# Optimization experiments

Measured on AMD Instinct MI355X. Metric: run time of the kernel, lower is better.

## Reference

```python
import jax, jax.numpy as jnp
import numpy as np

N, F, R, H, C = 16384, 128, 16, 8, 64
E = 163840
SELF_LOOP_FILL = 0.5
NEG_SLOPE = 0.2


def _glorot(key, shape):
    fan = shape[0] + shape[-1]
    lim = jnp.sqrt(6.0 / fan)
    return jax.random.uniform(key, shape, jnp.float32, -lim, lim)


def setup_inputs() -> dict:
    key = jax.random.key(0)
    ks = jax.random.split(key, 20)
    inp = {
        'x': jax.random.normal(ks[0], (N, F), jnp.float32),
        'edge_index': jax.random.randint(ks[1], (2, E), 0, N, jnp.int64),
        'edge_attr': jax.random.uniform(ks[2], (E, R), jnp.float32),
        # layer 1 (concat=True): in=F, out per head=C, heads=H
        'Wl1': _glorot(ks[3], (F, H * C)), 'bl1': jnp.zeros((H * C,), jnp.float32),
        'Wr1': _glorot(ks[4], (F, H * C)), 'br1': jnp.zeros((H * C,), jnp.float32),
        'We1': _glorot(ks[5], (R, H * C)),
        'att1': _glorot(ks[6], (H, C)),
        'bias1': jnp.zeros((H * C,), jnp.float32),
        # layer 2 (concat=False): in=H*C
        'Wl2': _glorot(ks[7], (H * C, H * C)), 'bl2': jnp.zeros((H * C,), jnp.float32),
        'Wr2': _glorot(ks[8], (H * C, H * C)), 'br2': jnp.zeros((H * C,), jnp.float32),
        'We2': _glorot(ks[9], (R, H * C)),
        'att2': _glorot(ks[10], (H, C)),
        'bias2': jnp.zeros((C,), jnp.float32),
    }
    return inp


def gatv2_layer(x, src, dst, e, Wl, bl, Wr, br, We, att, bias, concat):
    n = x.shape[0]
    h, c = att.shape
    xl = (x @ Wl + bl).reshape(n, h, c)   # source transform (used for messages)
    xr = (x @ Wr + br).reshape(n, h, c)   # target transform
    ep = (e @ We).reshape(-1, h, c)       # edge feature transform [E',H,C]
    z = jax.nn.leaky_relu(xl[src] + xr[dst] + ep, NEG_SLOPE)  # [E',H,C]
    logits = jnp.einsum('ehc,hc->eh', z, att)                 # [E',H]
    # softmax over incoming edges of each destination node
    m = jax.ops.segment_max(logits, dst, num_segments=n)
    m = jax.lax.stop_gradient(jnp.where(jnp.isfinite(m), m, 0.0))
    ex = jnp.exp(logits - m[dst])
    denom = jax.ops.segment_sum(ex, dst, num_segments=n)
    alpha = ex / (denom[dst] + 1e-16)                         # [E',H]
    out = jax.ops.segment_sum(xl[src] * alpha[..., None], dst, num_segments=n)  # [N,H,C]
    out = out.reshape(n, h * c) if concat else out.mean(axis=1)
    return out + bias


def reference(x, edge_index, edge_attr, Wl1, bl1, Wr1, br1, We1, att1, bias1,
              Wl2, bl2, Wr2, br2, We2, att2, bias2):
    n = x.shape[0]
    loops = jnp.arange(n, dtype=edge_index.dtype)
    src = jnp.concatenate([edge_index[0], loops])
    dst = jnp.concatenate([edge_index[1], loops])
    e = jnp.concatenate([edge_attr, jnp.full((n, edge_attr.shape[1]), SELF_LOOP_FILL, edge_attr.dtype)])
    out = gatv2_layer(x, src, dst, e, Wl1, bl1, Wr1, br1, We1, att1, bias1, concat=True)
    out = gatv2_layer(out, src, dst, e, Wl2, bl2, Wr2, br2, We2, att2, bias2, concat=False)
    return out
```

## Files before the change

### kernel.cpp

```cpp
#include <hip/hip_runtime.h>
#include <cstdint>

#define NN 16384
#define FF 128
#define RR 16
#define HH 8
#define CC 64
#define HC 512
#define NC 1024
#define EE 163840
#define ET (EE + NN)

typedef __attribute__((ext_vector_type(4))) float f32x4;
typedef __attribute__((ext_vector_type(8))) short short8;

__device__ __forceinline__ unsigned short f2bf(float f) {
  unsigned u = __builtin_bit_cast(unsigned, f);
  u = (u + 0x7FFFu + ((u >> 16) & 1u)) >> 16;
  return (unsigned short)u;
}
__device__ __forceinline__ float bf2f(unsigned short b) {
  unsigned u = ((unsigned)b) << 16;
  return __builtin_bit_cast(float, u);
}

__device__ __forceinline__ void gl_lds16(const void* g, void* l) {
  __builtin_amdgcn_global_load_lds(
      (const __attribute__((address_space(1))) unsigned int*)g,
      (__attribute__((address_space(3))) unsigned int*)l, 16, 0, 0);
}

__global__ __launch_bounds__(256) void count_kernel(const int* __restrict__ ei,
                                                    int* __restrict__ counts) {
  int e = blockIdx.x * 256 + threadIdx.x;
  if (e >= ET) return;
  int d = (e < EE) ? ei[EE + e] : (e - EE);
  atomicAdd(&counts[d], 1);
}

__global__ __launch_bounds__(1024) void scan_kernel(const int* __restrict__ counts,
                                                    int* __restrict__ offs,
                                                    int* __restrict__ cursor) {
  __shared__ int part[1024];
  int t = threadIdx.x;
  int base = t * 16;
  int loc[16];
  int s = 0;
#pragma unroll
  for (int i = 0; i < 16; ++i) { loc[i] = s; s += counts[base + i]; }
  part[t] = s;
  __syncthreads();
  for (int off = 1; off < 1024; off <<= 1) {
    int v = (t >= off) ? part[t - off] : 0;
    __syncthreads();
    part[t] += v;
    __syncthreads();
  }
  int excl = part[t] - s;
#pragma unroll
  for (int i = 0; i < 16; ++i) {
    int o = excl + loc[i];
    offs[base + i] = o;
    cursor[base + i] = o;
  }
  if (t == 1023) offs[NN] = part[1023];
}

__global__ __launch_bounds__(256) void scatter_kernel(const int* __restrict__ ei,
                                                      int* __restrict__ cursor,
                                                      int* __restrict__ csr,
                                                      int* __restrict__ srcc,
                                                      int* __restrict__ dstc) {
  int e = blockIdx.x * 256 + threadIdx.x;
  if (e >= ET) return;
  int s, d;
  if (e < EE) { s = ei[e]; d = ei[EE + e]; }
  else        { s = d = e - EE; }
  int p = atomicAdd(&cursor[d], 1);
  csr[p] = e;
  srcc[p] = s;
  dstc[p] = d;
}

__global__ __launch_bounds__(256) void pack_a_kernel(const float* __restrict__ A,
                                                     unsigned short* __restrict__ Ah,
                                                     unsigned short* __restrict__ Al,
                                                     int K) {
  int nkb = K >> 5;
  int rb = blockIdx.x / nkb, kb = blockIdx.x % nkb;
  int t = threadIdx.x;
  size_t obase = ((size_t)rb * nkb + kb) * 4096;
#pragma unroll
  for (int u = 0; u < 2; ++u) {
    int lin = t + u * 256;
    int r = lin >> 2, ch = lin & 3;
    int chs = (ch + (r >> 1)) & 3;
    const float* src = &A[(size_t)(rb * 128 + r) * K + kb * 32 + ch * 8];
    float4 v0 = *(const float4*)src;
    float4 v1 = *(const float4*)(src + 4);
    float v[8] = {v0.x, v0.y, v0.z, v0.w, v1.x, v1.y, v1.z, v1.w};
    short8 hv, lv;
#pragma unroll
    for (int j = 0; j < 8; ++j) {
      unsigned short h = f2bf(v[j]);
      unsigned short l = f2bf(v[j] - bf2f(h));
      hv[j] = (short)h; lv[j] = (short)l;
    }
    size_t o = obase + (size_t)r * 32 + chs * 8;
    *(short8*)&Ah[o] = hv;
    *(short8*)&Al[o] = lv;
  }
}

__global__ __launch_bounds__(256) void pack_w_kernel(const float* __restrict__ Wl,
                                                     const float* __restrict__ Wr,
                                                     unsigned short* __restrict__ Bh,
                                                     unsigned short* __restrict__ Bl,
                                                     int K) {
  int nkb = K >> 5;
  int nb = blockIdx.x / nkb, kb = blockIdx.x % nkb;
  int t = threadIdx.x;
  size_t obase = ((size_t)nb * nkb + kb) * 4096;
#pragma unroll
  for (int u = 0; u < 2; ++u) {
    int lin = t + u * 256;
    int n = lin >> 2, ch = lin & 3;
    int chs = (ch + (n >> 1)) & 3;
    int gn = nb * 128 + n;
    const float* W = (gn < HC) ? Wl : Wr;
    int cn = gn & (HC - 1);
    short8 hv, lv;
#pragma unroll
    for (int j = 0; j < 8; ++j) {
      float f = W[(size_t)(kb * 32 + ch * 8 + j) * HC + cn];
      unsigned short h = f2bf(f);
      unsigned short l = f2bf(f - bf2f(h));
      hv[j] = (short)h; lv[j] = (short)l;
    }
    size_t o = obase + (size_t)n * 32 + chs * 8;
    *(short8*)&Bh[o] = hv;
    *(short8*)&Bl[o] = lv;
  }
}

__global__ __launch_bounds__(256) void gemm_mfma_kernel(const unsigned short* __restrict__ Ah,
                                                        const unsigned short* __restrict__ Al,
                                                        const unsigned short* __restrict__ Bh,
                                                        const unsigned short* __restrict__ Bl,
                                                        const float* __restrict__ bl,
                                                        const float* __restrict__ br,
                                                        float* __restrict__ C, int K) {
  __shared__ unsigned short lAh[4096], lAl[4096], lBh[4096], lBl[4096];
  int tid = threadIdx.x;
  int wave = tid >> 6, lane = tid & 63;
  int l15 = lane & 15, quad = lane >> 4;
  int wm = wave >> 1, wn = wave & 1;
  int nb = blockIdx.x, rb = blockIdx.y;
  int nkb = K >> 5;

  const unsigned short* src = (wave == 0) ? Ah : (wave == 1) ? Al : (wave == 2) ? Bh : Bl;
  unsigned short* dst = (wave == 0) ? lAh : (wave == 1) ? lAl : (wave == 2) ? lBh : lBl;
  int blk = (wave < 2) ? rb : nb;
  size_t gstep = 4096;
  const unsigned short* gbase = src + ((size_t)blk * nkb) * gstep + lane * 8;

  f32x4 acc[4][4];
#pragma unroll
  for (int i = 0; i < 4; ++i)
#pragma unroll
    for (int j = 0; j < 4; ++j) acc[i][j] = (f32x4){0.f, 0.f, 0.f, 0.f};

  int offA[4], offB[4];
#pragma unroll
  for (int t = 0; t < 4; ++t) {
    int ra = wm * 64 + t * 16 + l15;
    offA[t] = ra * 32 + ((quad + (ra >> 1)) & 3) * 8;
    int rbn = wn * 64 + t * 16 + l15;
    offB[t] = rbn * 32 + ((quad + (rbn >> 1)) & 3) * 8;
  }

  for (int kb = 0; kb < nkb; ++kb) {
    const unsigned short* g = gbase + (size_t)kb * gstep;
#pragma unroll
    for (int i = 0; i < 8; ++i)
      gl_lds16(g + i * 512, dst + i * 512);
    __syncthreads();

    short8 ah[4], al_[4], bh[4], bl_[4];
#pragma unroll
    for (int t = 0; t < 4; ++t) {
      ah[t]  = *(const short8*)&lAh[offA[t]];
      al_[t] = *(const short8*)&lAl[offA[t]];
      bh[t]  = *(const short8*)&lBh[offB[t]];
      bl_[t] = *(const short8*)&lBl[offB[t]];
    }
#pragma unroll
    for (int tm = 0; tm < 4; ++tm)
#pragma unroll
      for (int tn = 0; tn < 4; ++tn) {
        acc[tm][tn] = __builtin_amdgcn_mfma_f32_16x16x32_bf16(ah[tm], bh[tn], acc[tm][tn], 0, 0, 0);
        acc[tm][tn] = __builtin_amdgcn_mfma_f32_16x16x32_bf16(ah[tm], bl_[tn], acc[tm][tn], 0, 0, 0);
        acc[tm][tn] = __builtin_amdgcn_mfma_f32_16x16x32_bf16(al_[tm], bh[tn], acc[tm][tn], 0, 0, 0);
      }
    __syncthreads();
  }

#pragma unroll
  for (int tm = 0; tm < 4; ++tm) {
    int row = rb * 128 + wm * 64 + tm * 16 + quad * 4;
#pragma unroll
    for (int tn = 0; tn < 4; ++tn) {
      int col = nb * 128 + wn * 64 + tn * 16 + l15;
      float bias = (col < HC) ? bl[col] : br[col - HC];
#pragma unroll
      for (int r = 0; r < 4; ++r)
        C[(size_t)(row + r) * NC + col] = acc[tm][tn][r] + bias;
    }
  }
}

__global__ __launch_bounds__(256, 4) void edge_logits_kernel(const int* __restrict__ csr,
                                                             const int* __restrict__ srcc,
                                                             const int* __restrict__ dstc,
                                                             const float* __restrict__ eattr,
                                                             const float* __restrict__ We,
                                                             const float* __restrict__ att,
                                                             const float* __restrict__ xlr,
                                                             float* __restrict__ logitsc) {
  __shared__ float se[64][16];
  __shared__ int ssrc[64];
  __shared__ int sdst[64];
  __shared__ int sedge[64];
  int t = threadIdx.x;
  int base = blockIdx.x * 64;
  int c0 = t * 2;
  float wf[RR][2];
#pragma unroll
  for (int r = 0; r < RR; ++r) {
    float2 w = *(const float2*)&We[r * HC + c0];
    wf[r][0] = w.x; wf[r][1] = w.y;
  }
  float2 amv = *(const float2*)&att[c0];
  if (t < 64) {
    int i = base + t;
    sedge[t] = csr[i];
    ssrc[t] = srcc[i];
    sdst[t] = dstc[i];
  }
  __syncthreads();
  {
    int k = t >> 2, r0 = (t & 3) * 4;
    int e = sedge[k];
    float4 v;
    if (e < EE) v = *(const float4*)&eattr[(size_t)e * RR + r0];
    else        v = make_float4(0.5f, 0.5f, 0.5f, 0.5f);
    se[k][r0 + 0] = v.x; se[k][r0 + 1] = v.y;
    se[k][r0 + 2] = v.z; se[k][r0 + 3] = v.w;
  }
  __syncthreads();
  int h = t >> 5;
#pragma unroll 2
  for (int k = 0; k < 64; ++k) {
    int s = ssrc[k], d = sdst[k];
    float2 lv = *(const float2*)&xlr[(size_t)s * NC + c0];
    float2 rv = *(const float2*)&xlr[(size_t)d * NC + HC + c0];
    const float4* sk = (const float4*)se[k];
    float4 e0 = sk[0], e1 = sk[1], e2 = sk[2], e3 = sk[3];
    float er[RR] = {e0.x, e0.y, e0.z, e0.w, e1.x, e1.y, e1.z, e1.w,
                    e2.x, e2.y, e2.z, e2.w, e3.x, e3.y, e3.z, e3.w};
    float ep0 = 0.f, ep1 = 0.f;
#pragma unroll
    for (int r = 0; r < RR; ++r) {
      ep0 = fmaf(er[r], wf[r][0], ep0);
      ep1 = fmaf(er[r], wf[r][1], ep1);
    }
    float z0 = lv.x + rv.x + ep0;
    float z1 = lv.y + rv.y + ep1;
    z0 = fmaf(0.2f, fminf(z0, 0.f), fmaxf(z0, 0.f));
    z1 = fmaf(0.2f, fminf(z1, 0.f), fmaxf(z1, 0.f));
    float p = fmaf(z0, amv.x, z1 * amv.y);
    p += __shfl_xor(p, 1);
    p += __shfl_xor(p, 2);
    p += __shfl_xor(p, 4);
    p += __shfl_xor(p, 8);
    p += __shfl_xor(p, 16);
    if ((t & 31) == 0) logitsc[(size_t)(base + k) * 8 + h] = p;
  }
}

__global__ __launch_bounds__(256) void softmax_kernel(const int* __restrict__ offs,
                                                      float* __restrict__ logitsc) {
  int lane = threadIdx.x & 63;
  int n = blockIdx.x * 4 + (threadIdx.x >> 6);
  int h = lane & 7, i0 = lane >> 3;
  int beg = offs[n], end = offs[n + 1];
  float m = -1e30f;
  for (int i = beg + i0; i < end; i += 8) m = fmaxf(m, logitsc[(size_t)i * 8 + h]);
  m = fmaxf(m, __shfl_xor(m, 8));
  m = fmaxf(m, __shfl_xor(m, 16));
  m = fmaxf(m, __shfl_xor(m, 32));
  float s = 0.f;
  for (int i = beg + i0; i < end; i += 8) {
    size_t idx = (size_t)i * 8 + h;
    float v = __expf(logitsc[idx] - m);
    logitsc[idx] = v;
    s += v;
  }
  s += __shfl_xor(s, 8);
  s += __shfl_xor(s, 16);
  s += __shfl_xor(s, 32);
  float inv = 1.f / (s + 1e-16f);
  for (int i = beg + i0; i < end; i += 8) {
    size_t idx = (size_t)i * 8 + h;
    logitsc[idx] *= inv;
  }
}

__global__ __launch_bounds__(256) void aggregate_concat_kernel(const int* __restrict__ srcc,
                                                               const int* __restrict__ offs,
                                                               const float* __restrict__ alphac,
                                                               const float* __restrict__ xlr,
                                                               const float* __restrict__ bias,
                                                               unsigned short* __restrict__ Ah2,
                                                               unsigned short* __restrict__ Al2) {
  int n = blockIdx.x, t = threadIdx.x;
  int beg = offs[n], end = offs[n + 1];
  int c0 = t, c1 = t + 256;
  int h0 = t >> 6, h1 = h0 + 4;
  float acc0 = 0.f, acc1 = 0.f;
#pragma unroll 2
  for (int i = beg; i < end; ++i) {
    int s = srcc[i];
    float a0 = alphac[(size_t)i * 8 + h0];
    float a1 = alphac[(size_t)i * 8 + h1];
    acc0 += a0 * xlr[(size_t)s * NC + c0];
    acc1 += a1 * xlr[(size_t)s * NC + c1];
  }
  float v0 = acc0 + bias[c0];
  float v1 = acc1 + bias[c1];
  int r = n & 127, rbk = n >> 7;
#pragma unroll
  for (int u = 0; u < 2; ++u) {
    int c = u ? c1 : c0;
    float v = u ? v1 : v0;
    int kb = c >> 5, ch = (c >> 3) & 3, j = c & 7;
    int chs = (ch + (r >> 1)) & 3;
    size_t idx = ((size_t)rbk * 16 + kb) * 4096 + (size_t)r * 32 + chs * 8 + j;
    unsigned short h = f2bf(v);
    Ah2[idx] = h;
    Al2[idx] = f2bf(v - bf2f(h));
  }
}

__global__ __launch_bounds__(256) void aggregate_mean_kernel(const int* __restrict__ srcc,
                                                             const int* __restrict__ offs,
                                                             const float* __restrict__ alphac,
                                                             const float* __restrict__ xlr,
                                                             const float* __restrict__ bias2,
                                                             float* __restrict__ out) {
  __shared__ float red[HC];
  int n = blockIdx.x, t = threadIdx.x;
  int beg = offs[n], end = offs[n + 1];
  int c0 = t, c1 = t + 256;
  int h0 = t >> 6, h1 = h0 + 4;
  float acc0 = 0.f, acc1 = 0.f;
#pragma unroll 2
  for (int i = beg; i < end; ++i) {
    int s = srcc[i];
    float a0 = alphac[(size_t)i * 8 + h0];
    float a1 = alphac[(size_t)i * 8 + h1];
    acc0 += a0 * xlr[(size_t)s * NC + c0];
    acc1 += a1 * xlr[(size_t)s * NC + c1];
  }
  red[c0] = acc0;
  red[c1] = acc1;
  __syncthreads();
  if (t < CC) {
    float ssum = 0.f;
#pragma unroll
    for (int hh = 0; hh < HH; ++hh) ssum += red[hh * CC + t];
    out[(size_t)n * CC + t] = ssum * 0.125f + bias2[t];
  }
}

extern "C" void kernel_launch(void* const* d_in, const int* in_sizes, int n_in,
                              void* d_out, int out_size, void* d_ws, size_t ws_size,
                              hipStream_t stream) {
  const float* x     = (const float*)d_in[0];
  const int*   ei    = (const int*)d_in[1];
  const float* eattr = (const float*)d_in[2];
  const float* Wl1   = (const float*)d_in[3];
  const float* bl1   = (const float*)d_in[4];
  const float* Wr1   = (const float*)d_in[5];
  const float* br1   = (const float*)d_in[6];
  const float* We1   = (const float*)d_in[7];
  const float* att1  = (const float*)d_in[8];
  const float* bias1 = (const float*)d_in[9];
  const float* Wl2   = (const float*)d_in[10];
  const float* bl2   = (const float*)d_in[11];
  const float* Wr2   = (const float*)d_in[12];
  const float* br2   = (const float*)d_in[13];
  const float* We2   = (const float*)d_in[14];
  const float* att2  = (const float*)d_in[15];
  const float* bias2 = (const float*)d_in[16];
  float* out = (float*)d_out;

  char* ws = (char*)d_ws;
  size_t off = 0;
  auto alloc = [&](size_t bytes) {
    char* p = ws + off;
    off += (bytes + 255) & ~(size_t)255;
    return p;
  };
  float* bufC = (float*)alloc((size_t)NN * NC * 4);
  float* logits = (float*)alloc((size_t)ET * HH * 4);
  unsigned short* Ah1 = (unsigned short*)alloc((size_t)NN * FF * 2);
  unsigned short* Al1 = (unsigned short*)alloc((size_t)NN * FF * 2);
  unsigned short* Ah2 = (unsigned short*)alloc((size_t)NN * HC * 2);
  unsigned short* Al2 = (unsigned short*)alloc((size_t)NN * HC * 2);
  unsigned short* Wh1 = (unsigned short*)alloc((size_t)FF * NC * 2);
  unsigned short* Wlo1 = (unsigned short*)alloc((size_t)FF * NC * 2);
  unsigned short* Wh2 = (unsigned short*)alloc((size_t)HC * NC * 2);
  unsigned short* Wlo2 = (unsigned short*)alloc((size_t)HC * NC * 2);
  int* counts = (int*)alloc((size_t)NN * 4);
  int* offs   = (int*)alloc((size_t)(NN + 1) * 4);
  int* cursor = (int*)alloc((size_t)NN * 4);
  int* csr    = (int*)alloc((size_t)ET * 4);
  int* srcc   = (int*)alloc((size_t)ET * 4);
  int* dstc   = (int*)alloc((size_t)ET * 4);
  (void)ws_size; (void)in_sizes; (void)n_in; (void)out_size;

  hipMemsetAsync(counts, 0, (size_t)NN * 4, stream);
  int eb = (ET + 255) / 256;
  count_kernel<<<eb, 256, 0, stream>>>(ei, counts);
  scan_kernel<<<1, 1024, 0, stream>>>(counts, offs, cursor);
  scatter_kernel<<<eb, 256, 0, stream>>>(ei, cursor, csr, srcc, dstc);

  pack_a_kernel<<<(NN / 128) * (FF / 32), 256, 0, stream>>>(x, Ah1, Al1, FF);
  pack_w_kernel<<<(NC / 128) * (FF / 32), 256, 0, stream>>>(Wl1, Wr1, Wh1, Wlo1, FF);
  pack_w_kernel<<<(NC / 128) * (HC / 32), 256, 0, stream>>>(Wl2, Wr2, Wh2, Wlo2, HC);

  dim3 ggrid(NC / 128, NN / 128);
  int elb = ET / 64;

  gemm_mfma_kernel<<<ggrid, 256, 0, stream>>>(Ah1, Al1, Wh1, Wlo1, bl1, br1, bufC, FF);
  edge_logits_kernel<<<elb, 256, 0, stream>>>(csr, srcc, dstc, eattr, We1, att1, bufC, logits);
  softmax_kernel<<<NN / 4, 256, 0, stream>>>(offs, logits);
  aggregate_concat_kernel<<<NN, 256, 0, stream>>>(srcc, offs, logits, bufC, bias1, Ah2, Al2);

  gemm_mfma_kernel<<<ggrid, 256, 0, stream>>>(Ah2, Al2, Wh2, Wlo2, bl2, br2, bufC, HC);
  edge_logits_kernel<<<elb, 256, 0, stream>>>(csr, srcc, dstc, eattr, We2, att2, bufC, logits);
  softmax_kernel<<<NN / 4, 256, 0, stream>>>(offs, logits);
  aggregate_mean_kernel<<<NN, 256, 0, stream>>>(srcc, offs, logits, bufC, bias2, out);
}
```

Baseline: 510.0 us.

## Compute edge feature projection with bf16x3 MFMA in edge logits kernel

```diff
diff --git a/kernel.cpp b/kernel.cpp
--- a/kernel.cpp
+++ b/kernel.cpp
@@ -143,6 +143,35 @@
   }
 }
 
+__global__ __launch_bounds__(256) void pack_ea_kernel(const float* __restrict__ eattr,
+                                                      unsigned short* __restrict__ Eh,
+                                                      unsigned short* __restrict__ El) {
+  size_t i8 = ((size_t)blockIdx.x * 256 + threadIdx.x) * 8;
+  float4 v0 = *(const float4*)&eattr[i8];
+  float4 v1 = *(const float4*)&eattr[i8 + 4];
+  float v[8] = {v0.x, v0.y, v0.z, v0.w, v1.x, v1.y, v1.z, v1.w};
+  short8 hv, lv;
+#pragma unroll
+  for (int j = 0; j < 8; ++j) {
+    unsigned short h = f2bf(v[j]);
+    hv[j] = (short)h;
+    lv[j] = (short)f2bf(v[j] - bf2f(h));
+  }
+  *(short8*)&Eh[i8] = hv;
+  *(short8*)&El[i8] = lv;
+}
+
+__global__ __launch_bounds__(256) void pack_we_kernel(const float* __restrict__ We,
+                                                      unsigned short* __restrict__ WhT,
+                                                      unsigned short* __restrict__ WlT) {
+  int i = blockIdx.x * 256 + threadIdx.x;
+  int c = i >> 4, r = i & 15;
+  float v = We[r * HC + c];
+  unsigned short h = f2bf(v);
+  WhT[i] = h;
+  WlT[i] = f2bf(v - bf2f(h));
+}
+
 __global__ __launch_bounds__(256) void gemm_mfma_kernel(const unsigned short* __restrict__ Ah,
                                                         const unsigned short* __restrict__ Al,
                                                         const unsigned short* __restrict__ Bh,
@@ -219,27 +248,28 @@
   }
 }
 
-__global__ __launch_bounds__(256, 4) void edge_logits_kernel(const int* __restrict__ csr,
-                                                             const int* __restrict__ srcc,
-                                                             const int* __restrict__ dstc,
-                                                             const float* __restrict__ eattr,
-                                                             const float* __restrict__ We,
-                                                             const float* __restrict__ att,
-                                                             const float* __restrict__ xlr,
-                                                             float* __restrict__ logitsc) {
-  __shared__ float se[64][16];
+__global__ __launch_bounds__(256, 4) void edge_logits_kernel(
+    const int* __restrict__ csr,
+    const int* __restrict__ srcc,
+    const int* __restrict__ dstc,
+    const unsigned short* __restrict__ EhT,
+    const unsigned short* __restrict__ ElT,
+    const unsigned short* __restrict__ WhT,
+    const unsigned short* __restrict__ WlT,
+    const float* __restrict__ att,
+    const float* __restrict__ xlr,
+    float* __restrict__ logitsc) {
+  __shared__ float ep[16][512];
   __shared__ int ssrc[64];
   __shared__ int sdst[64];
   __shared__ int sedge[64];
   int t = threadIdx.x;
   int base = blockIdx.x * 64;
   int c0 = t * 2;
-  float wf[RR][2];
-#pragma unroll
-  for (int r = 0; r < RR; ++r) {
-    float2 w = *(const float2*)&We[r * HC + c0];
-    wf[r][0] = w.x; wf[r][1] = w.y;
-  }
+  int lane = t & 63, wave = t >> 6;
+  int l15 = lane & 15, quad = lane >> 4;
+  int rbase = (quad & 1) * 8;
+  bool hiq = quad < 2;
   float2 amv = *(const float2*)&att[c0];
   if (t < 64) {
     int i = base + t;
@@ -247,44 +277,63 @@
     ssrc[t] = srcc[i];
     sdst[t] = dstc[i];
   }
-  __syncthreads();
-  {
-    int k = t >> 2, r0 = (t & 3) * 4;
-    int e = sedge[k];
-    float4 v;
-    if (e < EE) v = *(const float4*)&eattr[(size_t)e * RR + r0];
-    else        v = make_float4(0.5f, 0.5f, 0.5f, 0.5f);
-    se[k][r0 + 0] = v.x; se[k][r0 + 1] = v.y;
-    se[k][r0 + 2] = v.z; se[k][r0 + 3] = v.w;
+  const unsigned short* WT = hiq ? WhT : WlT;
+  short8 Bf[8];
+#pragma unroll
+  for (int i = 0; i < 8; ++i) {
+    int col = wave * 128 + i * 16 + l15;
+    Bf[i] = *(const short8*)&WT[col * 16 + rbase];
   }
   __syncthreads();
   int h = t >> 5;
-#pragma unroll 2
-  for (int k = 0; k < 64; ++k) {
-    int s = ssrc[k], d = sdst[k];
-    float2 lv = *(const float2*)&xlr[(size_t)s * NC + c0];
-    float2 rv = *(const float2*)&xlr[(size_t)d * NC + HC + c0];
-    const float4* sk = (const float4*)se[k];
-    float4 e0 = sk[0], e1 = sk[1], e2 = sk[2], e3 = sk[3];
-    float er[RR] = {e0.x, e0.y, e0.z, e0.w, e1.x, e1.y, e1.z, e1.w,
-                    e2.x, e2.y, e2.z, e2.w, e3.x, e3.y, e3.z, e3.w};
-    float ep0 = 0.f, ep1 = 0.f;
-#pragma unroll
-    for (int r = 0; r < RR; ++r) {
-      ep0 = fmaf(er[r], wf[r][0], ep0);
-      ep1 = fmaf(er[r], wf[r][1], ep1);
-    }
-    float z0 = lv.x + rv.x + ep0;
-    float z1 = lv.y + rv.y + ep1;
-    z0 = fmaf(0.2f, fminf(z0, 0.f), fmaxf(z0, 0.f));
-    z1 = fmaf(0.2f, fminf(z1, 0.f), fmaxf(z1, 0.f));
-    float p = fmaf(z0, amv.x, z1 * amv.y);
-    p += __shfl_xor(p, 1);
-    p += __shfl_xor(p, 2);
-    p += __shfl_xor(p, 4);
-    p += __shfl_xor(p, 8);
-    p += __shfl_xor(p, 16);
-    if ((t & 31) == 0) logitsc[(size_t)(base + k) * 8 + h] = p;
+  for (int chunk = 0; chunk < 4; ++chunk) {
+    int e = sedge[chunk * 16 + l15];
+    short8 A1, A2;
+    if (e < EE) {
+      A1 = *(const short8*)&EhT[(size_t)e * RR + rbase];
+    } else {
+#pragma unroll
+      for (int j = 0; j < 8; ++j) A1[j] = (short)0x3F00;
+    }
+    if (e < EE && hiq) {
+      A2 = *(const short8*)&ElT[(size_t)e * RR + rbase];
+    } else {
+#pragma unroll
+      for (int j = 0; j < 8; ++j) A2[j] = 0;
+    }
+    f32x4 acc[8];
+#pragma unroll
+    for (int i = 0; i < 8; ++i) acc[i] = (f32x4){0.f, 0.f, 0.f, 0.f};
+#pragma unroll
+    for (int i = 0; i < 8; ++i) {
+      acc[i] = __builtin_amdgcn_mfma_f32_16x16x32_bf16(A1, Bf[i], acc[i], 0, 0, 0);
+      acc[i] = __builtin_amdgcn_mfma_f32_16x16x32_bf16(A2, Bf[i], acc[i], 0, 0, 0);
+    }
+#pragma unroll
+    for (int i = 0; i < 8; ++i) {
+      int col = wave * 128 + i * 16 + l15;
+#pragma unroll
+      for (int r = 0; r < 4; ++r) ep[quad * 4 + r][col] = acc[i][r];
+    }
+#pragma unroll 4
+    for (int kk = 0; kk < 16; ++kk) {
+      int k = chunk * 16 + kk;
+      int s = ssrc[k], d = sdst[k];
+      float2 lv = *(const float2*)&xlr[(size_t)s * NC + c0];
+      float2 rv = *(const float2*)&xlr[(size_t)d * NC + HC + c0];
+      float2 epv = *(const float2*)&ep[kk][c0];
+      float z0 = lv.x + rv.x + epv.x;
+      float z1 = lv.y + rv.y + epv.y;
+      z0 = fmaf(0.2f, fminf(z0, 0.f), fmaxf(z0, 0.f));
+      z1 = fmaf(0.2f, fminf(z1, 0.f), fmaxf(z1, 0.f));
+      float p = fmaf(z0, amv.x, z1 * amv.y);
+      p += __shfl_xor(p, 1);
+      p += __shfl_xor(p, 2);
+      p += __shfl_xor(p, 4);
+      p += __shfl_xor(p, 8);
+      p += __shfl_xor(p, 16);
+      if ((t & 31) == 0) logitsc[(size_t)(base + k) * 8 + h] = p;
+    }
   }
 }
 
@@ -422,6 +471,12 @@
   unsigned short* Wlo1 = (unsigned short*)alloc((size_t)FF * NC * 2);
   unsigned short* Wh2 = (unsigned short*)alloc((size_t)HC * NC * 2);
   unsigned short* Wlo2 = (unsigned short*)alloc((size_t)HC * NC * 2);
+  unsigned short* EhT  = (unsigned short*)alloc((size_t)EE * RR * 2);
+  unsigned short* ElT  = (unsigned short*)alloc((size_t)EE * RR * 2);
+  unsigned short* Weh1 = (unsigned short*)alloc((size_t)HC * RR * 2);
+  unsigned short* Wel1 = (unsigned short*)alloc((size_t)HC * RR * 2);
+  unsigned short* Weh2 = (unsigned short*)alloc((size_t)HC * RR * 2);
+  unsigned short* Wel2 = (unsigned short*)alloc((size_t)HC * RR * 2);
   int* counts = (int*)alloc((size_t)NN * 4);
   int* offs   = (int*)alloc((size_t)(NN + 1) * 4);
   int* cursor = (int*)alloc((size_t)NN * 4);
@@ -439,17 +494,20 @@
   pack_a_kernel<<<(NN / 128) * (FF / 32), 256, 0, stream>>>(x, Ah1, Al1, FF);
   pack_w_kernel<<<(NC / 128) * (FF / 32), 256, 0, stream>>>(Wl1, Wr1, Wh1, Wlo1, FF);
   pack_w_kernel<<<(NC / 128) * (HC / 32), 256, 0, stream>>>(Wl2, Wr2, Wh2, Wlo2, HC);
+  pack_ea_kernel<<<(EE * RR) / (256 * 8), 256, 0, stream>>>(eattr, EhT, ElT);
+  pack_we_kernel<<<(HC * RR) / 256, 256, 0, stream>>>(We1, Weh1, Wel1);
+  pack_we_kernel<<<(HC * RR) / 256, 256, 0, stream>>>(We2, Weh2, Wel2);
 
   dim3 ggrid(NC / 128, NN / 128);
   int elb = ET / 64;
 
   gemm_mfma_kernel<<<ggrid, 256, 0, stream>>>(Ah1, Al1, Wh1, Wlo1, bl1, br1, bufC, FF);
-  edge_logits_kernel<<<elb, 256, 0, stream>>>(csr, srcc, dstc, eattr, We1, att1, bufC, logits);
+  edge_logits_kernel<<<elb, 256, 0, stream>>>(csr, srcc, dstc, EhT, ElT, Weh1, Wel1, att1, bufC, logits);
   softmax_kernel<<<NN / 4, 256, 0, stream>>>(offs, logits);
   aggregate_concat_kernel<<<NN, 256, 0, stream>>>(srcc, offs, logits, bufC, bias1, Ah2, Al2);
 
   gemm_mfma_kernel<<<ggrid, 256, 0, stream>>>(Ah2, Al2, Wh2, Wlo2, bl2, br2, bufC, HC);
-  edge_logits_kernel<<<elb, 256, 0, stream>>>(csr, srcc, dstc, eattr, We2, att2, bufC, logits);
+  edge_logits_kernel<<<elb, 256, 0, stream>>>(csr, srcc, dstc, EhT, ElT, Weh2, Wel2, att2, bufC, logits);
   softmax_kernel<<<NN / 4, 256, 0, stream>>>(offs, logits);
   aggregate_mean_kernel<<<NN, 256, 0, stream>>>(srcc, offs, logits, bufC, bias2, out);
 }
```

Result: slower. 576.1 us (+13.0%).
